# Optimization experiments

Hardware: AMD Instinct MI355X
Metric: run time of the kernel (lower is better)

## Reference

```python
import jax, jax.numpy as jnp
import numpy as np

B, L, D, DIN, A, V, R = 1024, 100, 256, 704, 128, 32000, 129


def setup_inputs() -> dict:
    key = jax.random.key(0)
    ks = jax.random.split(key, 18)
    s = 0.05
    inp = {
        "x": jax.random.normal(ks[0], (B, DIN), jnp.float32),
        "h0": jax.random.normal(ks[1], (B, D), jnp.float32),
        "c0": jax.random.normal(ks[2], (B, D), jnp.float32),
        "src_enc": jax.random.normal(ks[3], (B, L, D), jnp.float32),
        "src_token_ids": jax.random.randint(ks[4], (B, L), 0, V),
        "W_ih": jax.random.normal(ks[5], (4 * D, DIN), jnp.float32) * s,
        "b_ih": jax.random.normal(ks[6], (4 * D,), jnp.float32) * s,
        "W_hh": jax.random.normal(ks[7], (4 * D, D), jnp.float32) * s,
        "b_hh": jax.random.normal(ks[8], (4 * D,), jnp.float32) * s,
        "W_attn": jax.random.normal(ks[9], (D, D), jnp.float32) * s,
        "W_att_vec": jax.random.normal(ks[10], (A * 2, 2 * D), jnp.float32) * s,
        "W_ptr": jax.random.normal(ks[11], (D, D), jnp.float32) * s,
        "rule_emb": jax.random.normal(ks[12], (R, 128), jnp.float32) * s,
        "W_rule_proj": jax.random.normal(ks[13], (D, 128), jnp.float32) * s,
        "prim_emb": jax.random.normal(ks[14], (V, 128), jnp.float32) * s,
        "W_prim_proj": jax.random.normal(ks[15], (D, 128), jnp.float32) * s,
        "w_gen": jax.random.normal(ks[16], (2, D), jnp.float32) * s,
        "b_gen": jax.random.normal(ks[17], (2,), jnp.float32) * s,
    }
    # W_att_vec maps concat(h, ctx) [2D] -> ATT (=256); keep shape (256, 512)
    inp["W_att_vec"] = inp["W_att_vec"][:256]
    return inp


def reference(x, h0, c0, src_enc, src_token_ids, W_ih, b_ih, W_hh, b_hh,
              W_attn, W_att_vec, W_ptr, rule_emb, W_rule_proj,
              prim_emb, W_prim_proj, w_gen, b_gen):
    # --- LSTMCell (torch gate order i, f, g, o) ---
    gates = x @ W_ih.T + b_ih + h0 @ W_hh.T + b_hh          # [B, 4D]
    i, f, g, o = jnp.split(gates, 4, axis=-1)
    i, f, o = jax.nn.sigmoid(i), jax.nn.sigmoid(f), jax.nn.sigmoid(o)
    c = f * c0 + i * jnp.tanh(g)
    h = o * jnp.tanh(c)                                      # [B, D]

    # --- dot-product attention over source encodings ---
    enc_proj = src_enc @ W_attn.T                            # [B, L, D]
    scores = jnp.einsum('bd,bld->bl', h, enc_proj)
    alpha = jax.nn.softmax(scores, axis=-1)
    ctx = jnp.einsum('bl,bld->bd', alpha, src_enc)
    att = jnp.tanh(jnp.concatenate([h, ctx], axis=-1) @ W_att_vec.T)  # [B, 256]

    # --- apply-rule (production) readout ---
    rule_proj = rule_emb @ W_rule_proj.T                     # [R, 256]
    log_p_rule = jax.nn.log_softmax(att @ rule_proj.T, axis=-1)  # [B, R]

    # --- primitive generation readout ---
    prim_proj = prim_emb @ W_prim_proj.T                     # [V, 256]
    p_gen_prim = jax.nn.softmax(att @ prim_proj.T, axis=-1)  # [B, V]

    # --- pointer network copy distribution over source positions ---
    ptr_scores = jnp.einsum('bld,bd->bl', src_enc @ W_ptr.T, att)
    copy_p = jax.nn.softmax(ptr_scores, axis=-1)             # [B, L]

    # --- gen vs copy gate (softmax over 2, per usage in parse()) ---
    gate = jax.nn.softmax(att @ w_gen.T + b_gen, axis=-1)    # [B, 2]

    # --- combined primitive distribution: gen + scattered copy mass ---
    p_prim = gate[:, :1] * p_gen_prim                        # [B, V]
    copy_mass = gate[:, 1:] * copy_p                         # [B, L]
    bidx = jnp.arange(p_prim.shape[0])[:, None]
    p_prim = p_prim.at[bidx, src_token_ids].add(copy_mass)
    return log_p_rule, p_prim, h, c, att
```

## Files before the change

### kernel.cpp

```cpp
#include <hip/hip_runtime.h>
#include <hip/hip_bf16.h>
#include <math.h>

#define NB   1024
#define LL   100
#define DD   256
#define DINN 704
#define VV   32000
#define RR   129
#define KAV  512

typedef float f32x4 __attribute__((ext_vector_type(4)));
typedef short s16x8 __attribute__((ext_vector_type(8)));
typedef unsigned short u16;

__device__ __forceinline__ float sigf(float x) { return 1.0f / (1.0f + __expf(-x)); }

__device__ __forceinline__ u16 f2bf(float f) {
    unsigned int u = __float_as_uint(f);
    u += 0x7fffu + ((u >> 16) & 1u);
    return (u16)(u >> 16);
}
__device__ __forceinline__ float bf2f(u16 s) {
    return __uint_as_float(((unsigned int)s) << 16);
}

__global__ __launch_bounds__(256) void k_lstm(
    const float* __restrict__ x, const float* __restrict__ h0, const float* __restrict__ c0,
    const float* __restrict__ W_ih, const float* __restrict__ b_ih,
    const float* __restrict__ W_hh, const float* __restrict__ b_hh,
    float* __restrict__ out_h, float* __restrict__ out_c)
{
    __shared__ __align__(16) float As[16][36];
    __shared__ __align__(16) float Bs[16][68];
    __shared__ __align__(16) float gsm[32][68];
    const int t = threadIdx.x;
    const int row0 = blockIdx.x * 32;
    const int dg = blockIdx.y;
    const int tr = t >> 4, tc = t & 15;
    float acc[2][4] = {};

    for (int kt = 0; kt < 60; ++kt) {
        const float* __restrict__ Asrc;
        const float* __restrict__ Bsrc;
        int lda, kb;
        if (kt < 44) { Asrc = x;  Bsrc = W_ih; lda = DINN; kb = kt * 16; }
        else         { Asrc = h0; Bsrc = W_hh; lda = DD;   kb = (kt - 44) * 16; }
        __syncthreads();
#pragma unroll
        for (int p = 0; p < 2; ++p) {
            int e = t + p * 256;
            int r = e >> 4, kk = e & 15;
            As[kk][r] = Asrc[(row0 + r) * lda + kb + kk];
        }
#pragma unroll
        for (int p = 0; p < 4; ++p) {
            int e = t + p * 256;
// ... 8 lines not shown
            f32x4 b = *reinterpret_cast<const f32x4*>(&Bs[kk][tc * 4]);
#pragma unroll
            for (int i = 0; i < 4; ++i) {
                acc[0][i] = fmaf(a0, b[i], acc[0][i]);
                acc[1][i] = fmaf(a1, b[i], acc[1][i]);
            }
        }
    }
    __syncthreads();
#pragma unroll
    for (int j = 0; j < 2; ++j)
#pragma unroll
        for (int i = 0; i < 4; ++i)
            gsm[tr * 2 + j][tc * 4 + i] = acc[j][i];
    __syncthreads();

#pragma unroll
    for (int p = 0; p < 2; ++p) {
        int item = t + p * 256;
        int r = item >> 4, di = item & 15;
        int dcol = dg * 16 + di;
        float iv = gsm[r][di]      + b_ih[dcol]          + b_hh[dcol];
        float fv = gsm[r][16 + di] + b_ih[DD + dcol]     + b_hh[DD + dcol];
        float gv = gsm[r][32 + di] + b_ih[2 * DD + dcol] + b_hh[2 * DD + dcol];
        float ov = gsm[r][48 + di] + b_ih[3 * DD + dcol] + b_hh[3 * DD + dcol];
        float cprev = c0[(row0 + r) * DD + dcol];
        float cc = sigf(fv) * cprev + sigf(iv) * tanhf(gv);
        float hh = sigf(ov) * tanhf(cc);
        out_c[(row0 + r) * DD + dcol] = cc;
        out_h[(row0 + r) * DD + dcol] = hh;
    }
}

__global__ __launch_bounds__(256) void k_attn(
    const float* __restrict__ src_enc, const float* __restrict__ h,
    const float* __restrict__ W_attn, float* __restrict__ ctx_out)
{
    __shared__ __align__(16) u16 enc_s[LL * DD];
    __shared__ __align__(16) float h_s[DD];
    __shared__ __align__(16) float hw_s[DD];
    __shared__ float sc_s[LL];
    __shared__ float al_s[LL];
    const int b = blockIdx.x, t = threadIdx.x;
    const int lane = t & 63, w = t >> 6;

    h_s[t] = h[b * DD + t];
    __syncthreads();
    {
        float a0 = 0.f, a1 = 0.f, a2 = 0.f, a3 = 0.f;
        const float* __restrict__ wp = W_attn + t;
#pragma unroll 4
        for (int e = 0; e < DD; e += 4) {
            a0 = fmaf(h_s[e],     wp[(e)     * DD], a0);
            a1 = fmaf(h_s[e + 1], wp[(e + 1) * DD], a1);
            a2 = fmaf(h_s[e + 2], wp[(e + 2) * DD], a2);
            a3 = fmaf(h_s[e + 3], wp[(e + 3) * DD], a3);
        }
        hw_s[t] = (a0 + a1) + (a2 + a3);
    }
    __syncthreads();

    const float* __restrict__ enc = src_enc + (size_t)b * LL * DD;
    f32x4 hw4 = *reinterpret_cast<const f32x4*>(&hw_s[lane * 4]);

    for (int l = w; l < LL; l += 4) {
        f32x4 ev = *reinterpret_cast<const f32x4*>(&enc[l * DD + lane * 4]);
        float pr = hw4[0] * ev[0] + hw4[1] * ev[1] + hw4[2] * ev[2] + hw4[3] * ev[3];
#pragma unroll
        for (int m = 1; m < 64; m <<= 1) pr += __shfl_xor(pr, m);
        if (lane == 0) sc_s[l] = pr;
        u16* es = &enc_s[l * DD + lane * 4];
        es[0] = f2bf(ev[0]); es[1] = f2bf(ev[1]); es[2] = f2bf(ev[2]); es[3] = f2bf(ev[3]);
    }
    __syncthreads();
    if (w == 0) {
        float v0 = sc_s[lane];
        float v1 = (lane + 64 < LL) ? sc_s[lane + 64] : -1e30f;
        float m = fmaxf(v0, v1);
#pragma unroll
        for (int s = 1; s < 64; s <<= 1) m = fmaxf(m, __shfl_xor(m, s));
        float e0 = __expf(v0 - m);
        float e1 = (lane + 64 < LL) ? __expf(v1 - m) : 0.f;
        float ssum = e0 + e1;
#pragma unroll
        for (int s = 1; s < 64; s <<= 1) ssum += __shfl_xor(ssum, s);
        float inv = 1.f / ssum;
        al_s[lane] = e0 * inv;
        if (lane + 64 < LL) al_s[lane + 64] = e1 * inv;
    }
    __syncthreads();
    float accv = 0.f;
    for (int l = 0; l < LL; ++l) accv += al_s[l] * bf2f(enc_s[l * DD + t]);
    ctx_out[b * DD + t] = accv;
}

__global__ __launch_bounds__(256) void k_attvec(
    const float* __restrict__ h, const float* __restrict__ ctx,
    const float* __restrict__ W_att_vec, float* __restrict__ att_out)
{
    __shared__ __align__(16) float As[16][36];
    __shared__ __align__(16) float Bs[16][68];
    const int t = threadIdx.x;
    const int row0 = blockIdx.x * 32;
    const int col0 = blockIdx.y * 64;
    const int tr = t >> 4, tc = t & 15;
    float acc[2][4] = {};
    for (int kt = 0; kt < 32; ++kt) {
        const float* __restrict__ Asrc = (kt < 16) ? h : ctx;
        int kb = (kt < 16) ? kt * 16 : (kt - 16) * 16;
        int kg = kt * 16;
        __syncthreads();
#pragma unroll
        for (int p = 0; p < 2; ++p) {
            int e = t + p * 256;
            int r = e >> 4, kk = e & 15;
            As[kk][r] = Asrc[(row0 + r) * DD + kb + kk];
        }
#pragma unroll
        for (int p = 0; p < 4; ++p) {
            int e = t + p * 256;
            int r = e >> 4, kk = e & 15;
            Bs[kk][r] = W_att_vec[(col0 + r) * KAV + kg + kk];
        }
        __syncthreads();
#pragma unroll
        for (int kk = 0; kk < 16; ++kk) {
            float a0 = As[kk][tr * 2], a1 = As[kk][tr * 2 + 1];
            f32x4 b = *reinterpret_cast<const f32x4*>(&Bs[kk][tc * 4]);
#pragma unroll
            for (int i = 0; i < 4; ++i) {
                acc[0][i] = fmaf(a0, b[i], acc[0][i]);
                acc[1][i] = fmaf(a1, b[i], acc[1][i]);
            }
        }
    }
#pragma unroll
    for (int j = 0; j < 2; ++j)
#pragma unroll
        for (int i = 0; i < 4; ++i)
            att_out[(row0 + tr * 2 + j) * DD + col0 + tc * 4 + i] = tanhf(acc[j][i]);
}

__global__ __launch_bounds__(256) void k_readout(
    const float* __restrict__ att, const float* __restrict__ src_enc,
    const float* __restrict__ rule_proj, const float* __restrict__ W_ptr,
    const float* __restrict__ W_prim_proj, const float* __restrict__ w_gen,
    const float* __restrict__ b_gen,
    float* __restrict__ log_p_rule, u16* __restrict__ att_bf,
    float* __restrict__ gate0_ws, float* __restrict__ copy_mass)
{
    __shared__ __align__(16) float att_s[DD];
    __shared__ __align__(16) float atw_s[DD];
    __shared__ float red_s[RR];
    __shared__ float sc_s[LL];
    __shared__ float gl_s[2];
    __shared__ float mS[2];
    const int b = blockIdx.x, t = threadIdx.x;
    const int lane = t & 63, w = t >> 6;
    att_s[t] = att[b * DD + t];
    __syncthreads();

    if (t < RR) {
        float acc = 0.f;
        const float* __restrict__ rp = &rule_proj[t * DD];
        for (int d = 0; d < DD; d += 4) {
            f32x4 r4 = *reinterpret_cast<const f32x4*>(&rp[d]);
            f32x4 a4 = *reinterpret_cast<const f32x4*>(&att_s[d]);
            acc += r4[0] * a4[0] + r4[1] * a4[1] + r4[2] * a4[2] + r4[3] * a4[3];
        }
        red_s[t] = acc;
    }
    {
        float aw = 0.f;
        for (int d = 0; d < DD; ++d) aw += att_s[d] * W_ptr[d * DD + t];
        atw_s[t] = aw;
    }
    if (t < 128) {
        float ap = 0.f;
        for (int d = 0; d < DD; ++d) ap += att_s[d] * W_prim_proj[d * 128 + t];
        att_bf[b * 128 + t] = f2bf(ap);
    }
    if (w < 2) {
        f32x4 a4 = *reinterpret_cast<const f32x4*>(&att_s[lane * 4]);
        f32x4 g4 = *reinterpret_cast<const f32x4*>(&w_gen[w * DD + lane * 4]);
        float p = a4[0] * g4[0] + a4[1] * g4[1] + a4[2] * g4[2] + a4[3] * g4[3];
#pragma unroll
        for (int s = 1; s < 64; s <<= 1) p += __shfl_xor(p, s);
        if (lane == 0) gl_s[w] = p + b_gen[w];
    }
    __syncthreads();

    if (w == 0) {
        float v0 = red_s[lane];
        float v1 = red_s[lane + 64];
        float v2 = (lane == 0) ? red_s[128] : -1e30f;
        float m = fmaxf(fmaxf(v0, v1), v2);
#pragma unroll
        for (int s = 1; s < 64; s <<= 1) m = fmaxf(m, __shfl_xor(m, s));
        float ssum = __expf(v0 - m) + __expf(v1 - m) + ((lane == 0) ? __expf(v2 - m) : 0.f);
#pragma unroll
        for (int s = 1; s < 64; s <<= 1) ssum += __shfl_xor(ssum, s);
        if (lane == 0) { mS[0] = m; mS[1] = logf(ssum); }
    }
    __syncthreads();
    if (t < RR) log_p_rule[b * RR + t] = red_s[t] - mS[0] - mS[1];

    float g0 = gl_s[0], g1 = gl_s[1];
    float gm = fmaxf(g0, g1);
    float e0 = __expf(g0 - gm), e1 = __expf(g1 - gm);
    float gate1 = e1 / (e0 + e1);
    if (t == 0) gate0_ws[b] = e0 / (e0 + e1);

    const float* __restrict__ enc = src_enc + (size_t)b * LL * DD;
    f32x4 aw4 = *reinterpret_cast<const f32x4*>(&atw_s[lane * 4]);
    for (int l = w; l < LL; l += 4) {
        f32x4 ev = *reinterpret_cast<const f32x4*>(&enc[l * DD + lane * 4]);
        float pr = aw4[0] * ev[0] + aw4[1] * ev[1] + aw4[2] * ev[2] + aw4[3] * ev[3];
#pragma unroll
        for (int m = 1; m < 64; m <<= 1) pr += __shfl_xor(pr, m);
        if (lane == 0) sc_s[l] = pr;
    }
    __syncthreads();
    if (w == 0) {
        float v0 = sc_s[lane];
        float v1 = (lane + 64 < LL) ? sc_s[lane + 64] : -1e30f;
        float m = fmaxf(v0, v1);
#pragma unroll
        for (int s = 1; s < 64; s <<= 1) m = fmaxf(m, __shfl_xor(m, s));
        float ee0 = __expf(v0 - m);
        float ee1 = (lane + 64 < LL) ? __expf(v1 - m) : 0.f;
        float ssum = ee0 + ee1;
#pragma unroll
        for (int s = 1; s < 64; s <<= 1) ssum += __shfl_xor(ssum, s);
        float inv = 1.f / ssum;
        copy_mass[b * LL + lane] = gate1 * ee0 * inv;
        if (lane + 64 < LL) copy_mass[b * LL + lane + 64] = gate1 * ee1 * inv;
    }
}

__global__ __launch_bounds__(256) void k_conv(
    const float* __restrict__ src, u16* __restrict__ dst,
    const float* __restrict__ rule_emb, const float* __restrict__ W_rule_proj,
    float* __restrict__ rule_proj)
{
    __shared__ float re_s[128];
    const int bx = blockIdx.x, t = threadIdx.x;
    if (bx < RR && t < 128) re_s[t] = rule_emb[bx * 128 + t];

    int i = (bx * 256 + t) * 8;
    f32x4 a = *reinterpret_cast<const f32x4*>(&src[i]);
    f32x4 b = *reinterpret_cast<const f32x4*>(&src[i + 4]);
    s16x8 r;
    r[0] = (short)f2bf(a[0]); r[1] = (short)f2bf(a[1]);
    r[2] = (short)f2bf(a[2]); r[3] = (short)f2bf(a[3]);
    r[4] = (short)f2bf(b[0]); r[5] = (short)f2bf(b[1]);
    r[6] = (short)f2bf(b[2]); r[7] = (short)f2bf(b[3]);
    *reinterpret_cast<s16x8*>(&dst[i]) = r;

    if (bx < RR) {
        __syncthreads();
        float acc = 0.f;
        const float* __restrict__ wr = &W_rule_proj[t * 128];
#pragma unroll 8
        for (int k = 0; k < 128; k += 4) {
            f32x4 w4 = *reinterpret_cast<const f32x4*>(&wr[k]);
            acc += w4[0] * re_s[k] + w4[1] * re_s[k + 1]
                 + w4[2] * re_s[k + 2] + w4[3] * re_s[k + 3];
        }
        rule_proj[bx * DD + t] = acc;
    }
}

template <int PASS>
__global__ __launch_bounds__(256) void k_prim(
    const u16* __restrict__ att_bf, const u16* __restrict__ prim_bf,
    const float* __restrict__ coef, float* __restrict__ stats, float* __restrict__ p_prim)
{
    const int t = threadIdx.x;
    const int lane = t & 63, w = t >> 6;
    const int lm = lane & 15, lq = lane >> 4;
    const int colbase = blockIdx.x * 128 + (w & 1) * 64;
    const int chunk = colbase >> 6;
    const int rowblk = blockIdx.y * 256;

    s16x8 pfr[4][4];
#pragma unroll
    for (int kg = 0; kg < 4; ++kg)
#pragma unroll
        for (int mg = 0; mg < 4; ++mg)
            pfr[kg][mg] = *reinterpret_cast<const s16x8*>(
                &prim_bf[(size_t)(colbase + mg * 16 + lm) * 128 + kg * 32 + lq * 8]);

    for (int it = 0; it < 2; ++it) {
        const int rowbase = rowblk + it * 128 + (w >> 1) * 64;
        f32x4 acc[4][4] = {};
#pragma unroll
        for (int kg = 0; kg < 4; ++kg) {
            s16x8 afr[4];
#pragma unroll
            for (int ng = 0; ng < 4; ++ng)
                afr[ng] = *reinterpret_cast<const s16x8*>(
                    &att_bf[(rowbase + ng * 16 + lm) * 128 + kg * 32 + lq * 8]);
// ... 62 lines not shown
}

extern "C" void kernel_launch(void* const* d_in, const int* in_sizes, int n_in,
                              void* d_out, int out_size, void* d_ws, size_t ws_size,
                              hipStream_t stream)
{
    const float* x         = (const float*)d_in[0];
    const float* h0        = (const float*)d_in[1];
    const float* c0        = (const float*)d_in[2];
    const float* src_enc   = (const float*)d_in[3];
    const int*   tok       = (const int*)  d_in[4];
    const float* W_ih      = (const float*)d_in[5];
    const float* b_ih      = (const float*)d_in[6];
    const float* W_hh      = (const float*)d_in[7];
    const float* b_hh      = (const float*)d_in[8];
    const float* W_attn    = (const float*)d_in[9];
    const float* W_att_vec = (const float*)d_in[10];
    const float* W_ptr     = (const float*)d_in[11];
    const float* rule_emb  = (const float*)d_in[12];
    const float* W_rule_pr = (const float*)d_in[13];
    const float* prim_emb  = (const float*)d_in[14];
    const float* W_prim_pr = (const float*)d_in[15];
    const float* w_gen     = (const float*)d_in[16];
    const float* b_gen     = (const float*)d_in[17];

    float* out    = (float*)d_out;
    float* o_logp = out;
    float* o_pp   = out + 1024 * 129;
    float* o_h    = o_pp + (size_t)1024 * 32000;
    float* o_c    = o_h + 1024 * 256;
    float* o_att  = o_c + 1024 * 256;

    float* wsf      = (float*)d_ws;
    float* ws_ctx   = wsf;
    float* ws_rp    = ws_ctx   + 262144;
    float* ws_gate  = ws_rp    + 33280;
    float* ws_cm    = ws_gate  + 1024;
    float* ws_coef  = ws_cm    + 102400;
    float* ws_stats = ws_coef  + 1024;
    u16*   ws_attbf = (u16*)(ws_stats + 512000);
    u16*   ws_primbf= (u16*)(ws_stats + 512000 + 65536);

    k_conv<<<dim3(2000), 256, 0, stream>>>(prim_emb, ws_primbf, rule_emb, W_rule_pr, ws_rp);
    k_lstm<<<dim3(32, 16), 256, 0, stream>>>(x, h0, c0, W_ih, b_ih, W_hh, b_hh, o_h, o_c);
    k_attn<<<dim3(1024), 256, 0, stream>>>(src_enc, o_h, W_attn, ws_ctx);
    k_attvec<<<dim3(32, 4), 256, 0, stream>>>(o_h, ws_ctx, W_att_vec, o_att);
    k_readout<<<dim3(1024), 256, 0, stream>>>(o_att, src_enc, ws_rp, W_ptr, W_prim_pr,
                                              w_gen, b_gen, o_logp, ws_attbf, ws_gate, ws_cm);
    k_prim<0><<<dim3(250, 4), 256, 0, stream>>>(ws_attbf, ws_primbf, nullptr, ws_stats, nullptr);
    k_combine<<<dim3(4), 256, 0, stream>>>(ws_stats, ws_gate, ws_coef);
    k_prim<1><<<dim3(250, 4), 256, 0, stream>>>(ws_attbf, ws_primbf, ws_coef, nullptr, o_pp);
    k_scatter<<<dim3(400), 256, 0, stream>>>(tok, ws_cm, o_pp);
}
```

Baseline: 267.4 us.

## Fuse attention, att-vector projection and readout into one per-batch kernel

Merges k_attn, k_attvec and k_readout into a single per-row kernel. It computes the context vector, the att-vector GEMV, the pointer, prim and rule projections, and the copy softmax while keeping intermediates in shared memory. W_att_vec is pre-transposed by extra blocks appended to k_conv so the per-row GEMV reads are coalesced. The bf16 staging of src_enc in LDS is dropped, and the second and third passes re-read src_enc from global/L2. This saves two launches and the ctx round-trip, but the att-vector projection becomes a per-row GEMV that re-reads the weights for each batch row instead of a tiled GEMM.

```diff
diff --git a/kernel.cpp b/kernel.cpp
--- a/kernel.cpp
+++ b/kernel.cpp
@@ -11,6 +11,7 @@
 #define KAV  512
 
 typedef float f32x4 __attribute__((ext_vector_type(4)));
+typedef float f32x2 __attribute__((ext_vector_type(2)));
 typedef short s16x8 __attribute__((ext_vector_type(8)));
 typedef unsigned short u16;
 
@@ -20,9 +21,6 @@
     unsigned int u = __float_as_uint(f);
     u += 0x7fffu + ((u >> 16) & 1u);
     return (u16)(u >> 16);
-}
-__device__ __forceinline__ float bf2f(u16 s) {
-    return __uint_as_float(((unsigned int)s) << 16);
 }
 
 __global__ __launch_bounds__(256) void k_lstm(
@@ -97,219 +95,31 @@
     }
 }
 
-__global__ __launch_bounds__(256) void k_attn(
-    const float* __restrict__ src_enc, const float* __restrict__ h,
-    const float* __restrict__ W_attn, float* __restrict__ ctx_out)
-{
-    __shared__ __align__(16) u16 enc_s[LL * DD];
-    __shared__ __align__(16) float h_s[DD];
-    __shared__ __align__(16) float hw_s[DD];
-    __shared__ float sc_s[LL];
-    __shared__ float al_s[LL];
-    const int b = blockIdx.x, t = threadIdx.x;
-    const int lane = t & 63, w = t >> 6;
-
-    h_s[t] = h[b * DD + t];
-    __syncthreads();
-    {
-        float a0 = 0.f, a1 = 0.f, a2 = 0.f, a3 = 0.f;
-        const float* __restrict__ wp = W_attn + t;
-#pragma unroll 4
-        for (int e = 0; e < DD; e += 4) {
-            a0 = fmaf(h_s[e],     wp[(e)     * DD], a0);
-            a1 = fmaf(h_s[e + 1], wp[(e + 1) * DD], a1);
-            a2 = fmaf(h_s[e + 2], wp[(e + 2) * DD], a2);
-            a3 = fmaf(h_s[e + 3], wp[(e + 3) * DD], a3);
-        }
-        hw_s[t] = (a0 + a1) + (a2 + a3);
-    }
-    __syncthreads();
-
-    const float* __restrict__ enc = src_enc + (size_t)b * LL * DD;
-    f32x4 hw4 = *reinterpret_cast<const f32x4*>(&hw_s[lane * 4]);
-
-    for (int l = w; l < LL; l += 4) {
-        f32x4 ev = *reinterpret_cast<const f32x4*>(&enc[l * DD + lane * 4]);
-        float pr = hw4[0] * ev[0] + hw4[1] * ev[1] + hw4[2] * ev[2] + hw4[3] * ev[3];
-#pragma unroll
-        for (int m = 1; m < 64; m <<= 1) pr += __shfl_xor(pr, m);
-        if (lane == 0) sc_s[l] = pr;
-        u16* es = &enc_s[l * DD + lane * 4];
-        es[0] = f2bf(ev[0]); es[1] = f2bf(ev[1]); es[2] = f2bf(ev[2]); es[3] = f2bf(ev[3]);
-    }
-    __syncthreads();
-    if (w == 0) {
-        float v0 = sc_s[lane];
-        float v1 = (lane + 64 < LL) ? sc_s[lane + 64] : -1e30f;
-        float m = fmaxf(v0, v1);
-#pragma unroll
-        for (int s = 1; s < 64; s <<= 1) m = fmaxf(m, __shfl_xor(m, s));
-        float e0 = __expf(v0 - m);
-        float e1 = (lane + 64 < LL) ? __expf(v1 - m) : 0.f;
-        float ssum = e0 + e1;
-#pragma unroll
-        for (int s = 1; s < 64; s <<= 1) ssum += __shfl_xor(ssum, s);
-        float inv = 1.f / ssum;
-        al_s[lane] = e0 * inv;
-        if (lane + 64 < LL) al_s[lane + 64] = e1 * inv;
-    }
-    __syncthreads();
-    float accv = 0.f;
-    for (int l = 0; l < LL; ++l) accv += al_s[l] * bf2f(enc_s[l * DD + t]);
-    ctx_out[b * DD + t] = accv;
-}
-
-__global__ __launch_bounds__(256) void k_attvec(
-    const float* __restrict__ h, const float* __restrict__ ctx,
-    const float* __restrict__ W_att_vec, float* __restrict__ att_out)
-{
-    __shared__ __align__(16) float As[16][36];
-    __shared__ __align__(16) float Bs[16][68];
-    const int t = threadIdx.x;
-    const int row0 = blockIdx.x * 32;
-    const int col0 = blockIdx.y * 64;
-    const int tr = t >> 4, tc = t & 15;
-    float acc[2][4] = {};
-    for (int kt = 0; kt < 32; ++kt) {
-        const float* __restrict__ Asrc = (kt < 16) ? h : ctx;
-        int kb = (kt < 16) ? kt * 16 : (kt - 16) * 16;
-        int kg = kt * 16;
-        __syncthreads();
-#pragma unroll
-        for (int p = 0; p < 2; ++p) {
-            int e = t + p * 256;
-            int r = e >> 4, kk = e & 15;
-            As[kk][r] = Asrc[(row0 + r) * DD + kb + kk];
-        }
-#pragma unroll
-        for (int p = 0; p < 4; ++p) {
-            int e = t + p * 256;
-            int r = e >> 4, kk = e & 15;
-            Bs[kk][r] = W_att_vec[(col0 + r) * KAV + kg + kk];
-        }
-        __syncthreads();
-#pragma unroll
-        for (int kk = 0; kk < 16; ++kk) {
-            float a0 = As[kk][tr * 2], a1 = As[kk][tr * 2 + 1];
-            f32x4 b = *reinterpret_cast<const f32x4*>(&Bs[kk][tc * 4]);
-#pragma unroll
-            for (int i = 0; i < 4; ++i) {
-                acc[0][i] = fmaf(a0, b[i], acc[0][i]);
-                acc[1][i] = fmaf(a1, b[i], acc[1][i]);
-            }
-        }
-    }
-#pragma unroll
-    for (int j = 0; j < 2; ++j)
-#pragma unroll
-        for (int i = 0; i < 4; ++i)
-            att_out[(row0 + tr * 2 + j) * DD + col0 + tc * 4 + i] = tanhf(acc[j][i]);
-}
-
-__global__ __launch_bounds__(256) void k_readout(
-    const float* __restrict__ att, const float* __restrict__ src_enc,
-    const float* __restrict__ rule_proj, const float* __restrict__ W_ptr,
-    const float* __restrict__ W_prim_proj, const float* __restrict__ w_gen,
-    const float* __restrict__ b_gen,
-    float* __restrict__ log_p_rule, u16* __restrict__ att_bf,
-    float* __restrict__ gate0_ws, float* __restrict__ copy_mass)
-{
-    __shared__ __align__(16) float att_s[DD];
-    __shared__ __align__(16) float atw_s[DD];
-    __shared__ float red_s[RR];
-    __shared__ float sc_s[LL];
-    __shared__ float gl_s[2];
-    __shared__ float mS[2];
-    const int b = blockIdx.x, t = threadIdx.x;
-    const int lane = t & 63, w = t >> 6;
-    att_s[t] = att[b * DD + t];
-    __syncthreads();
-
-    if (t < RR) {
-        float acc = 0.f;
-        const float* __restrict__ rp = &rule_proj[t * DD];
-        for (int d = 0; d < DD; d += 4) {
-            f32x4 r4 = *reinterpret_cast<const f32x4*>(&rp[d]);
-            f32x4 a4 = *reinterpret_cast<const f32x4*>(&att_s[d]);
-            acc += r4[0] * a4[0] + r4[1] * a4[1] + r4[2] * a4[2] + r4[3] * a4[3];
-        }
-        red_s[t] = acc;
-    }
-    {
-        float aw = 0.f;
-        for (int d = 0; d < DD; ++d) aw += att_s[d] * W_ptr[d * DD + t];
-        atw_s[t] = aw;
-    }
-    if (t < 128) {
-        float ap = 0.f;
-        for (int d = 0; d < DD; ++d) ap += att_s[d] * W_prim_proj[d * 128 + t];
-        att_bf[b * 128 + t] = f2bf(ap);
-    }
-    if (w < 2) {
-        f32x4 a4 = *reinterpret_cast<const f32x4*>(&att_s[lane * 4]);
-        f32x4 g4 = *reinterpret_cast<const f32x4*>(&w_gen[w * DD + lane * 4]);
-        float p = a4[0] * g4[0] + a4[1] * g4[1] + a4[2] * g4[2] + a4[3] * g4[3];
-#pragma unroll
-        for (int s = 1; s < 64; s <<= 1) p += __shfl_xor(p, s);
-        if (lane == 0) gl_s[w] = p + b_gen[w];
-    }
-    __syncthreads();
-
-    if (w == 0) {
-        float v0 = red_s[lane];
-        float v1 = red_s[lane + 64];
-        float v2 = (lane == 0) ? red_s[128] : -1e30f;
-        float m = fmaxf(fmaxf(v0, v1), v2);
-#pragma unroll
-        for (int s = 1; s < 64; s <<= 1) m = fmaxf(m, __shfl_xor(m, s));
-        float ssum = __expf(v0 - m) + __expf(v1 - m) + ((lane == 0) ? __expf(v2 - m) : 0.f);
-#pragma unroll
-        for (int s = 1; s < 64; s <<= 1) ssum += __shfl_xor(ssum, s);
-        if (lane == 0) { mS[0] = m; mS[1] = logf(ssum); }
-    }
-    __syncthreads();
-    if (t < RR) log_p_rule[b * RR + t] = red_s[t] - mS[0] - mS[1];
-
-    float g0 = gl_s[0], g1 = gl_s[1];
-    float gm = fmaxf(g0, g1);
-    float e0 = __expf(g0 - gm), e1 = __expf(g1 - gm);
-    float gate1 = e1 / (e0 + e1);
-    if (t == 0) gate0_ws[b] = e0 / (e0 + e1);
-
-    const float* __restrict__ enc = src_enc + (size_t)b * LL * DD;
-    f32x4 aw4 = *reinterpret_cast<const f32x4*>(&atw_s[lane * 4]);
-    for (int l = w; l < LL; l += 4) {
-        f32x4 ev = *reinterpret_cast<const f32x4*>(&enc[l * DD + lane * 4]);
-        float pr = aw4[0] * ev[0] + aw4[1] * ev[1] + aw4[2] * ev[2] + aw4[3] * ev[3];
-#pragma unroll
-        for (int m = 1; m < 64; m <<= 1) pr += __shfl_xor(pr, m);
-        if (lane == 0) sc_s[l] = pr;
-    }
-    __syncthreads();
-    if (w == 0) {
-        float v0 = sc_s[lane];
-        float v1 = (lane + 64 < LL) ? sc_s[lane + 64] : -1e30f;
-        float m = fmaxf(v0, v1);
-#pragma unroll
-        for (int s = 1; s < 64; s <<= 1) m = fmaxf(m, __shfl_xor(m, s));
-        float ee0 = __expf(v0 - m);
-        float ee1 = (lane + 64 < LL) ? __expf(v1 - m) : 0.f;
-        float ssum = ee0 + ee1;
-#pragma unroll
-        for (int s = 1; s < 64; s <<= 1) ssum += __shfl_xor(ssum, s);
-        float inv = 1.f / ssum;
-        copy_mass[b * LL + lane] = gate1 * ee0 * inv;
-        if (lane + 64 < LL) copy_mass[b * LL + lane + 64] = gate1 * ee1 * inv;
-    }
-}
-
 __global__ __launch_bounds__(256) void k_conv(
     const float* __restrict__ src, u16* __restrict__ dst,
     const float* __restrict__ rule_emb, const float* __restrict__ W_rule_proj,
-    float* __restrict__ rule_proj)
+    float* __restrict__ rule_proj,
+    const float* __restrict__ W_att_vec, float* __restrict__ wt)
 {
     __shared__ float re_s[128];
+    __shared__ __align__(16) float tile[64][65];
     const int bx = blockIdx.x, t = threadIdx.x;
+
+    if (bx >= 2000) {
+        const int id = bx - 2000;
+        const int c0 = (id >> 3) * 64;
+        const int k0 = (id & 7) * 64;
+        const int r = t >> 6, cc = t & 63;
+#pragma unroll
+        for (int p = 0; p < 16; ++p)
+            tile[r + p * 4][cc] = W_att_vec[(c0 + r + p * 4) * KAV + k0 + cc];
+        __syncthreads();
+#pragma unroll
+        for (int p = 0; p < 16; ++p)
+            wt[(k0 + r + p * 4) * DD + c0 + cc] = tile[cc][r + p * 4];
+        return;
+    }
+
     if (bx < RR && t < 128) re_s[t] = rule_emb[bx * 128 + t];
 
     int i = (bx * 256 + t) * 8;
@@ -333,6 +143,223 @@
                  + w4[2] * re_s[k + 2] + w4[3] * re_s[k + 3];
         }
         rule_proj[bx * DD + t] = acc;
+    }
+}
+
+__global__ __launch_bounds__(256) void k_fused(
+    const float* __restrict__ src_enc, const float* __restrict__ h,
+    const float* __restrict__ W_attn, const float* __restrict__ Wt,
+    const float* __restrict__ rule_proj, const float* __restrict__ W_ptr,
+    const float* __restrict__ W_prim_proj, const float* __restrict__ w_gen,
+    const float* __restrict__ b_gen,
+    float* __restrict__ att_out, float* __restrict__ log_p_rule,
+    u16* __restrict__ att_bf, float* __restrict__ gate0_ws,
+    float* __restrict__ copy_mass)
+{
+    __shared__ __align__(16) float hc_s[2 * DD];
+    __shared__ __align__(16) float att_s[DD];
+    __shared__ __align__(16) float part[4][DD];
+    __shared__ __align__(16) float partp[4][128];
+    __shared__ float sc_s[LL];
+    __shared__ float al_s[LL];
+    __shared__ float red_s[RR];
+    __shared__ float gl_s[2];
+    __shared__ float mS[2];
+
+    const int b = blockIdx.x, t = threadIdx.x;
+    const int lane = t & 63, w = t >> 6;
+    const float* __restrict__ enc = src_enc + (size_t)b * LL * DD;
+
+    hc_s[t] = h[b * DD + t];
+    __syncthreads();
+
+    {
+        f32x4 p = {0.f, 0.f, 0.f, 0.f};
+        const int e0 = w * 64;
+#pragma unroll 4
+        for (int e = e0; e < e0 + 64; ++e) {
+            float hv = hc_s[e];
+            f32x4 wv = *reinterpret_cast<const f32x4*>(&W_attn[e * DD + lane * 4]);
+            p[0] = fmaf(hv, wv[0], p[0]); p[1] = fmaf(hv, wv[1], p[1]);
+            p[2] = fmaf(hv, wv[2], p[2]); p[3] = fmaf(hv, wv[3], p[3]);
+        }
+        *reinterpret_cast<f32x4*>(&part[w][lane * 4]) = p;
+    }
+    __syncthreads();
+    f32x4 hw4;
+    {
+        f32x4 p0 = *reinterpret_cast<const f32x4*>(&part[0][lane * 4]);
+        f32x4 p1 = *reinterpret_cast<const f32x4*>(&part[1][lane * 4]);
+        f32x4 p2 = *reinterpret_cast<const f32x4*>(&part[2][lane * 4]);
+        f32x4 p3 = *reinterpret_cast<const f32x4*>(&part[3][lane * 4]);
+        hw4[0] = (p0[0] + p1[0]) + (p2[0] + p3[0]);
+        hw4[1] = (p0[1] + p1[1]) + (p2[1] + p3[1]);
+        hw4[2] = (p0[2] + p1[2]) + (p2[2] + p3[2]);
+        hw4[3] = (p0[3] + p1[3]) + (p2[3] + p3[3]);
+    }
+
+    for (int l = w; l < LL; l += 4) {
+        f32x4 ev = *reinterpret_cast<const f32x4*>(&enc[l * DD + lane * 4]);
+        float pr = hw4[0] * ev[0] + hw4[1] * ev[1] + hw4[2] * ev[2] + hw4[3] * ev[3];
+#pragma unroll
+        for (int m = 1; m < 64; m <<= 1) pr += __shfl_xor(pr, m);
+        if (lane == 0) sc_s[l] = pr;
+    }
+    __syncthreads();
+    if (w == 0) {
+        float v0 = sc_s[lane];
+        float v1 = (lane + 64 < LL) ? sc_s[lane + 64] : -1e30f;
+        float m = fmaxf(v0, v1);
+#pragma unroll
+        for (int s = 1; s < 64; s <<= 1) m = fmaxf(m, __shfl_xor(m, s));
+        float e0 = __expf(v0 - m);
+        float e1 = (lane + 64 < LL) ? __expf(v1 - m) : 0.f;
+        float ssum = e0 + e1;
+#pragma unroll
+        for (int s = 1; s < 64; s <<= 1) ssum += __shfl_xor(ssum, s);
+        float inv = 1.f / ssum;
+        al_s[lane] = e0 * inv;
+        if (lane + 64 < LL) al_s[lane + 64] = e1 * inv;
+    }
+    __syncthreads();
+
+    {
+        float a0 = 0.f, a1 = 0.f, a2 = 0.f, a3 = 0.f;
+        for (int l = 0; l < LL; l += 4) {
+            a0 = fmaf(al_s[l],     enc[(l)     * DD + t], a0);
+            a1 = fmaf(al_s[l + 1], enc[(l + 1) * DD + t], a1);
+            a2 = fmaf(al_s[l + 2], enc[(l + 2) * DD + t], a2);
+            a3 = fmaf(al_s[l + 3], enc[(l + 3) * DD + t], a3);
+        }
+        hc_s[DD + t] = (a0 + a1) + (a2 + a3);
+    }
+    __syncthreads();
+
+    {
+        f32x4 p = {0.f, 0.f, 0.f, 0.f};
+        const int gk0 = w * 128;
+#pragma unroll 4
+        for (int kk = 0; kk < 128; ++kk) {
+            float cv = hc_s[gk0 + kk];
+            f32x4 wv = *reinterpret_cast<const f32x4*>(&Wt[(gk0 + kk) * DD + lane * 4]);
+            p[0] = fmaf(cv, wv[0], p[0]); p[1] = fmaf(cv, wv[1], p[1]);
+            p[2] = fmaf(cv, wv[2], p[2]); p[3] = fmaf(cv, wv[3], p[3]);
+        }
+        *reinterpret_cast<f32x4*>(&part[w][lane * 4]) = p;
+    }
+    __syncthreads();
+    {
+        float av = (part[0][t] + part[1][t]) + (part[2][t] + part[3][t]);
+        av = tanhf(av);
+        att_s[t] = av;
+        att_out[b * DD + t] = av;
+    }
+    __syncthreads();
+
+    {
+        f32x4 p = {0.f, 0.f, 0.f, 0.f};
+        const int e0 = w * 64;
+#pragma unroll 4
+        for (int e = e0; e < e0 + 64; ++e) {
+            float av = att_s[e];
+            f32x4 wv = *reinterpret_cast<const f32x4*>(&W_ptr[e * DD + lane * 4]);
+            p[0] = fmaf(av, wv[0], p[0]); p[1] = fmaf(av, wv[1], p[1]);
+            p[2] = fmaf(av, wv[2], p[2]); p[3] = fmaf(av, wv[3], p[3]);
+        }
+        *reinterpret_cast<f32x4*>(&part[w][lane * 4]) = p;
+    }
+    {
+        float p0 = 0.f, p1 = 0.f;
+        const int e0 = w * 64;
+#pragma unroll 4
+        for (int e = e0; e < e0 + 64; ++e) {
+            float av = att_s[e];
+            f32x2 wv = *reinterpret_cast<const f32x2*>(&W_prim_proj[e * 128 + lane * 2]);
+            p0 = fmaf(av, wv[0], p0);
+            p1 = fmaf(av, wv[1], p1);
+        }
+        partp[w][lane * 2]     = p0;
+        partp[w][lane * 2 + 1] = p1;
+    }
+    if (t < RR) {
+        float acc = 0.f;
+        const float* __restrict__ rp = &rule_proj[t * DD];
+#pragma unroll 4
+        for (int d = 0; d < DD; d += 4) {
+            f32x4 r4 = *reinterpret_cast<const f32x4*>(&rp[d]);
+            f32x4 a4 = *reinterpret_cast<const f32x4*>(&att_s[d]);
+            acc += r4[0] * a4[0] + r4[1] * a4[1] + r4[2] * a4[2] + r4[3] * a4[3];
+        }
+        red_s[t] = acc;
+    }
+    if (w < 2) {
+        f32x4 a4 = *reinterpret_cast<const f32x4*>(&att_s[lane * 4]);
+        f32x4 g4 = *reinterpret_cast<const f32x4*>(&w_gen[w * DD + lane * 4]);
+        float p = a4[0] * g4[0] + a4[1] * g4[1] + a4[2] * g4[2] + a4[3] * g4[3];
+#pragma unroll
+        for (int s = 1; s < 64; s <<= 1) p += __shfl_xor(p, s);
+        if (lane == 0) gl_s[w] = p + b_gen[w];
+    }
+    __syncthreads();
+
+    f32x4 aw4;
+    {
+        f32x4 p0 = *reinterpret_cast<const f32x4*>(&part[0][lane * 4]);
+        f32x4 p1 = *reinterpret_cast<const f32x4*>(&part[1][lane * 4]);
+        f32x4 p2 = *reinterpret_cast<const f32x4*>(&part[2][lane * 4]);
+        f32x4 p3 = *reinterpret_cast<const f32x4*>(&part[3][lane * 4]);
+        aw4[0] = (p0[0] + p1[0]) + (p2[0] + p3[0]);
+        aw4[1] = (p0[1] + p1[1]) + (p2[1] + p3[1]);
+        aw4[2] = (p0[2] + p1[2]) + (p2[2] + p3[2]);
+        aw4[3] = (p0[3] + p1[3]) + (p2[3] + p3[3]);
+    }
+    if (t < 128) {
+        float ap = (partp[0][t] + partp[1][t]) + (partp[2][t] + partp[3][t]);
+        att_bf[b * 128 + t] = f2bf(ap);
+    }
+    if (w == 0) {
+        float v0 = red_s[lane];
+        float v1 = red_s[lane + 64];
+        float v2 = (lane == 0) ? red_s[128] : -1e30f;
+        float m = fmaxf(fmaxf(v0, v1), v2);
+#pragma unroll
+        for (int s = 1; s < 64; s <<= 1) m = fmaxf(m, __shfl_xor(m, s));
+        float ssum = __expf(v0 - m) + __expf(v1 - m) + ((lane == 0) ? __expf(v2 - m) : 0.f);
+#pragma unroll
+        for (int s = 1; s < 64; s <<= 1) ssum += __shfl_xor(ssum, s);
+        if (lane == 0) { mS[0] = m; mS[1] = logf(ssum); }
+    }
+    __syncthreads();
+    if (t < RR) log_p_rule[b * RR + t] = red_s[t] - mS[0] - mS[1];
+
+    float g0 = gl_s[0], g1 = gl_s[1];
+    float gm = fmaxf(g0, g1);
+    float e0g = __expf(g0 - gm), e1g = __expf(g1 - gm);
+    float gate1 = e1g / (e0g + e1g);
+    if (t == 0) gate0_ws[b] = e0g / (e0g + e1g);
+
+    for (int l = w; l < LL; l += 4) {
+        f32x4 ev = *reinterpret_cast<const f32x4*>(&enc[l * DD + lane * 4]);
+        float pr = aw4[0] * ev[0] + aw4[1] * ev[1] + aw4[2] * ev[2] + aw4[3] * ev[3];
+#pragma unroll
+        for (int m = 1; m < 64; m <<= 1) pr += __shfl_xor(pr, m);
+        if (lane == 0) sc_s[l] = pr;
+    }
+    __syncthreads();
+    if (w == 0) {
+        float v0 = sc_s[lane];
+        float v1 = (lane + 64 < LL) ? sc_s[lane + 64] : -1e30f;
+        float m = fmaxf(v0, v1);
+#pragma unroll
+        for (int s = 1; s < 64; s <<= 1) m = fmaxf(m, __shfl_xor(m, s));
+        float ee0 = __expf(v0 - m);
+        float ee1 = (lane + 64 < LL) ? __expf(v1 - m) : 0.f;
+        float ssum = ee0 + ee1;
+#pragma unroll
+        for (int s = 1; s < 64; s <<= 1) ssum += __shfl_xor(ssum, s);
+        float inv = 1.f / ssum;
+        copy_mass[b * LL + lane] = gate1 * ee0 * inv;
+        if (lane + 64 < LL) copy_mass[b * LL + lane + 64] = gate1 * ee1 * inv;
     }
 }
 
@@ -461,21 +488,21 @@
     float* o_att  = o_c + 1024 * 256;
 
     float* wsf      = (float*)d_ws;
-    float* ws_ctx   = wsf;
-    float* ws_rp    = ws_ctx   + 262144;
+    float* ws_rp    = wsf;
     float* ws_gate  = ws_rp    + 33280;
     float* ws_cm    = ws_gate  + 1024;
     float* ws_coef  = ws_cm    + 102400;
     float* ws_stats = ws_coef  + 1024;
-    u16*   ws_attbf = (u16*)(ws_stats + 512000);
-    u16*   ws_primbf= (u16*)(ws_stats + 512000 + 65536);
-
-    k_conv<<<dim3(2000), 256, 0, stream>>>(prim_emb, ws_primbf, rule_emb, W_rule_pr, ws_rp);
+    float* ws_wt    = ws_stats + 512000;
+    u16*   ws_attbf = (u16*)(ws_wt + 131072);
+    u16*   ws_primbf= (u16*)(ws_wt + 131072 + 65536);
+
+    k_conv<<<dim3(2032), 256, 0, stream>>>(prim_emb, ws_primbf, rule_emb, W_rule_pr,
+                                           ws_rp, W_att_vec, ws_wt);
     k_lstm<<<dim3(32, 16), 256, 0, stream>>>(x, h0, c0, W_ih, b_ih, W_hh, b_hh, o_h, o_c);
-    k_attn<<<dim3(1024), 256, 0, stream>>>(src_enc, o_h, W_attn, ws_ctx);
-    k_attvec<<<dim3(32, 4), 256, 0, stream>>>(o_h, ws_ctx, W_att_vec, o_att);
-    k_readout<<<dim3(1024), 256, 0, stream>>>(o_att, src_enc, ws_rp, W_ptr, W_prim_pr,
-                                              w_gen, b_gen, o_logp, ws_attbf, ws_gate, ws_cm);
+    k_fused<<<dim3(1024), 256, 0, stream>>>(src_enc, o_h, W_attn, ws_wt, ws_rp, W_ptr,
+                                            W_prim_pr, w_gen, b_gen,
+                                            o_att, o_logp, ws_attbf, ws_gate, ws_cm);
     k_prim<0><<<dim3(250, 4), 256, 0, stream>>>(ws_attbf, ws_primbf, nullptr, ws_stats, nullptr);
     k_combine<<<dim3(4), 256, 0, stream>>>(ws_stats, ws_gate, ws_coef);
     k_prim<1><<<dim3(250, 4), 256, 0, stream>>>(ws_attbf, ws_primbf, ws_coef, nullptr, o_pp);
```

New measurement: 249.8 us. -6.6%, faster.

## Batch per-row matvecs into tiled GEMMs and restructure attention kernel

Applied to the files above, without the earlier changes.

The per-batch-row matrix-vector products (h·W_attn, att·W_ptr, att·W_prim_proj) move out of the per-row kernels into tiled GEMM kernels, so each weight tile is reused across 32 rows instead of being reread by every block. The attention kernel now stages the bf16 encodings in padded shared memory first, then computes scores and the context with a split-over-L reduction. The readout splits into a rule/gate kernel and a pointer kernel. This adds extra launches and workspace round trips in exchange for removing redundant weight traffic.

```diff
diff --git a/kernel.cpp b/kernel.cpp
--- a/kernel.cpp
+++ b/kernel.cpp
@@ -9,20 +9,23 @@
 #define VV   32000
 #define RR   129
 #define KAV  512
+#define ROWU 129
 
 typedef float f32x4 __attribute__((ext_vector_type(4)));
+typedef float f32x2 __attribute__((ext_vector_type(2)));
 typedef short s16x8 __attribute__((ext_vector_type(8)));
 typedef unsigned short u16;
+typedef unsigned int u32;
 
 __device__ __forceinline__ float sigf(float x) { return 1.0f / (1.0f + __expf(-x)); }
 
 __device__ __forceinline__ u16 f2bf(float f) {
-    unsigned int u = __float_as_uint(f);
+    u32 u = __float_as_uint(f);
     u += 0x7fffu + ((u >> 16) & 1u);
     return (u16)(u >> 16);
 }
 __device__ __forceinline__ float bf2f(u16 s) {
-    return __uint_as_float(((unsigned int)s) << 16);
+    return __uint_as_float(((u32)s) << 16);
 }
 
 __global__ __launch_bounds__(256) void k_lstm(
@@ -97,47 +100,132 @@
     }
 }
 
-__global__ __launch_bounds__(256) void k_attn(
-    const float* __restrict__ src_enc, const float* __restrict__ h,
-    const float* __restrict__ W_attn, float* __restrict__ ctx_out)
-{
-    __shared__ __align__(16) u16 enc_s[LL * DD];
-    __shared__ __align__(16) float h_s[DD];
+__global__ __launch_bounds__(256) void k_conv(
+    const float* __restrict__ src, u16* __restrict__ dst,
+    const float* __restrict__ rule_emb, const float* __restrict__ W_rule_proj,
+    float* __restrict__ rule_proj)
+{
+    __shared__ float re_s[128];
+    const int bx = blockIdx.x, t = threadIdx.x;
+
+    if (bx < RR && t < 128) re_s[t] = rule_emb[bx * 128 + t];
+
+    int i = (bx * 256 + t) * 8;
+    f32x4 a = *reinterpret_cast<const f32x4*>(&src[i]);
+    f32x4 b = *reinterpret_cast<const f32x4*>(&src[i + 4]);
+    s16x8 r;
+    r[0] = (short)f2bf(a[0]); r[1] = (short)f2bf(a[1]);
+    r[2] = (short)f2bf(a[2]); r[3] = (short)f2bf(a[3]);
+    r[4] = (short)f2bf(b[0]); r[5] = (short)f2bf(b[1]);
+    r[6] = (short)f2bf(b[2]); r[7] = (short)f2bf(b[3]);
+    *reinterpret_cast<s16x8*>(&dst[i]) = r;
+
+    if (bx < RR) {
+        __syncthreads();
+        float acc = 0.f;
+        const float* __restrict__ wr = &W_rule_proj[t * 128];
+#pragma unroll 8
+        for (int k = 0; k < 128; k += 4) {
+            f32x4 w4 = *reinterpret_cast<const f32x4*>(&wr[k]);
+            acc += w4[0] * re_s[k] + w4[1] * re_s[k + 1]
+                 + w4[2] * re_s[k + 2] + w4[3] * re_s[k + 3];
+        }
+        rule_proj[bx * DD + t] = acc;
+    }
+}
+
+__global__ __launch_bounds__(256) void k_hw(
+    const float* __restrict__ h, const float* __restrict__ W_attn, float* __restrict__ hW)
+{
+    __shared__ __align__(16) float As[16][36];
+    __shared__ __align__(16) float Bs[16][68];
+    const int t = threadIdx.x;
+    const int row0 = blockIdx.x * 32;
+    const int col0 = blockIdx.y * 64;
+    const int tr = t >> 4, tc = t & 15;
+    float acc[2][4] = {};
+    for (int kt = 0; kt < 16; ++kt) {
+        __syncthreads();
+#pragma unroll
+        for (int p = 0; p < 2; ++p) {
+            int e = t + p * 256;
+            int r = e >> 4, kk = e & 15;
+            As[kk][r] = h[(row0 + r) * DD + kt * 16 + kk];
+        }
+#pragma unroll
+        for (int p = 0; p < 4; ++p) {
+            int e = t + p * 256;
+            int kk = e >> 6, c = e & 63;
+            Bs[kk][c] = W_attn[(kt * 16 + kk) * DD + col0 + c];
+        }
+        __syncthreads();
+#pragma unroll
+        for (int kk = 0; kk < 16; ++kk) {
+            float a0 = As[kk][tr * 2], a1 = As[kk][tr * 2 + 1];
+            f32x4 b = *reinterpret_cast<const f32x4*>(&Bs[kk][tc * 4]);
+#pragma unroll
+            for (int i = 0; i < 4; ++i) {
+                acc[0][i] = fmaf(a0, b[i], acc[0][i]);
+                acc[1][i] = fmaf(a1, b[i], acc[1][i]);
+            }
+        }
+    }
+#pragma unroll
+    for (int j = 0; j < 2; ++j) {
+        f32x4 v;
+#pragma unroll
+        for (int i = 0; i < 4; ++i) v[i] = acc[j][i];
+        *reinterpret_cast<f32x4*>(&hW[(row0 + tr * 2 + j) * DD + col0 + tc * 4]) = v;
+    }
+}
+
+__global__ __launch_bounds__(256) void k_attn2(
+    const float* __restrict__ src_enc, const float* __restrict__ hW,
+    float* __restrict__ ctx_out)
+{
+    __shared__ u32 enc_u[LL * ROWU];
+    __shared__ __align__(16) float part[4][DD];
     __shared__ __align__(16) float hw_s[DD];
     __shared__ float sc_s[LL];
     __shared__ float al_s[LL];
+
     const int b = blockIdx.x, t = threadIdx.x;
     const int lane = t & 63, w = t >> 6;
-
-    h_s[t] = h[b * DD + t];
-    __syncthreads();
+    const float* __restrict__ enc = src_enc + (size_t)b * LL * DD;
+
+    hw_s[t] = hW[b * DD + t];
+
+#pragma unroll 5
+    for (int p = 0; p < 25; ++p) {
+        int q = p * 256 + t;
+        int l = q >> 6, dq = q & 63;
+        f32x4 ev = *reinterpret_cast<const f32x4*>(&enc[l * DD + dq * 4]);
+        u32 w0 = (u32)f2bf(ev[0]) | ((u32)f2bf(ev[1]) << 16);
+        u32 w1 = (u32)f2bf(ev[2]) | ((u32)f2bf(ev[3]) << 16);
+        enc_u[l * ROWU + dq * 2]     = w0;
+        enc_u[l * ROWU + dq * 2 + 1] = w1;
+    }
+    __syncthreads();
+
     {
-        float a0 = 0.f, a1 = 0.f, a2 = 0.f, a3 = 0.f;
-        const float* __restrict__ wp = W_attn + t;
-#pragma unroll 4
-        for (int e = 0; e < DD; e += 4) {
-            a0 = fmaf(h_s[e],     wp[(e)     * DD], a0);
-            a1 = fmaf(h_s[e + 1], wp[(e + 1) * DD], a1);
-            a2 = fmaf(h_s[e + 2], wp[(e + 2) * DD], a2);
-            a3 = fmaf(h_s[e + 3], wp[(e + 3) * DD], a3);
-        }
-        hw_s[t] = (a0 + a1) + (a2 + a3);
-    }
-    __syncthreads();
-
-    const float* __restrict__ enc = src_enc + (size_t)b * LL * DD;
-    f32x4 hw4 = *reinterpret_cast<const f32x4*>(&hw_s[lane * 4]);
-
-    for (int l = w; l < LL; l += 4) {
-        f32x4 ev = *reinterpret_cast<const f32x4*>(&enc[l * DD + lane * 4]);
-        float pr = hw4[0] * ev[0] + hw4[1] * ev[1] + hw4[2] * ev[2] + hw4[3] * ev[3];
-#pragma unroll
-        for (int m = 1; m < 64; m <<= 1) pr += __shfl_xor(pr, m);
-        if (lane == 0) sc_s[l] = pr;
-        u16* es = &enc_s[l * DD + lane * 4];
-        es[0] = f2bf(ev[0]); es[1] = f2bf(ev[1]); es[2] = f2bf(ev[2]); es[3] = f2bf(ev[3]);
-    }
-    __syncthreads();
+        const int sl = ((w >> 1) << 6) + lane;
+        float sp = 0.f;
+        if (sl < LL) {
+            const u32* __restrict__ rp = enc_u + sl * ROWU + ((w & 1) << 6);
+            const float* __restrict__ hp = hw_s + ((w & 1) << 7);
+#pragma unroll 16
+            for (int k = 0; k < 64; ++k) {
+                u32 v = rp[k];
+                sp = fmaf(bf2f((u16)v),         hp[2 * k],     sp);
+                sp = fmaf(bf2f((u16)(v >> 16)), hp[2 * k + 1], sp);
+            }
+        }
+        part[w][lane] = sp;
+    }
+    __syncthreads();
+    if (t < LL) sc_s[t] = part[(t >> 6) << 1][t & 63] + part[((t >> 6) << 1) + 1][t & 63];
+    __syncthreads();
+
     if (w == 0) {
         float v0 = sc_s[lane];
         float v1 = (lane + 64 < LL) ? sc_s[lane + 64] : -1e30f;
@@ -154,12 +242,29 @@
         if (lane + 64 < LL) al_s[lane + 64] = e1 * inv;
     }
     __syncthreads();
-    float accv = 0.f;
-    for (int l = 0; l < LL; ++l) accv += al_s[l] * bf2f(enc_s[l * DD + t]);
-    ctx_out[b * DD + t] = accv;
-}
-
-__global__ __launch_bounds__(256) void k_attvec(
+
+    {
+        const int l0 = w * 25;
+        float c0 = 0.f, c1 = 0.f, c2 = 0.f, c3 = 0.f;
+#pragma unroll 5
+        for (int li = 0; li < 25; ++li) {
+            int l = l0 + li;
+            float a = al_s[l];
+            u32 v0 = enc_u[l * ROWU + lane * 2];
+            u32 v1 = enc_u[l * ROWU + lane * 2 + 1];
+            c0 = fmaf(a, bf2f((u16)v0), c0);
+            c1 = fmaf(a, bf2f((u16)(v0 >> 16)), c1);
+            c2 = fmaf(a, bf2f((u16)v1), c2);
+            c3 = fmaf(a, bf2f((u16)(v1 >> 16)), c3);
+        }
+        f32x4 p; p[0] = c0; p[1] = c1; p[2] = c2; p[3] = c3;
+        *reinterpret_cast<f32x4*>(&part[w][lane * 4]) = p;
+    }
+    __syncthreads();
+    ctx_out[b * DD + t] = (part[0][t] + part[1][t]) + (part[2][t] + part[3][t]);
+}
+
+__global__ __launch_bounds__(256) void k_att(
     const float* __restrict__ h, const float* __restrict__ ctx,
     const float* __restrict__ W_att_vec, float* __restrict__ att_out)
 {
@@ -206,18 +311,71 @@
             att_out[(row0 + tr * 2 + j) * DD + col0 + tc * 4 + i] = tanhf(acc[j][i]);
 }
 
-__global__ __launch_bounds__(256) void k_readout(
-    const float* __restrict__ att, const float* __restrict__ src_enc,
-    const float* __restrict__ rule_proj, const float* __restrict__ W_ptr,
-    const float* __restrict__ W_prim_proj, const float* __restrict__ w_gen,
-    const float* __restrict__ b_gen,
-    float* __restrict__ log_p_rule, u16* __restrict__ att_bf,
-    float* __restrict__ gate0_ws, float* __restrict__ copy_mass)
+__global__ __launch_bounds__(256) void k_ptrproj(
+    const float* __restrict__ att, const float* __restrict__ W_ptr,
+    const float* __restrict__ W_prim_proj,
+    float* __restrict__ atw, u16* __restrict__ att_bf)
+{
+    __shared__ __align__(16) float As[16][36];
+    __shared__ __align__(16) float Bs[16][68];
+    const int t = threadIdx.x;
+    const int row0 = blockIdx.x * 32;
+    const int col0 = blockIdx.y * 64;
+    const int tr = t >> 4, tc = t & 15;
+    float acc[2][4] = {};
+    for (int kt = 0; kt < 16; ++kt) {
+        __syncthreads();
+#pragma unroll
+        for (int p = 0; p < 2; ++p) {
+            int e = t + p * 256;
+            int r = e >> 4, kk = e & 15;
+            As[kk][r] = att[(row0 + r) * DD + kt * 16 + kk];
+        }
+#pragma unroll
+        for (int p = 0; p < 4; ++p) {
+            int e = t + p * 256;
+            int kk = e >> 6, c = e & 63;
+            Bs[kk][c] = (col0 < 256)
+                ? W_ptr[(kt * 16 + kk) * DD + col0 + c]
+                : W_prim_proj[(kt * 16 + kk) * 128 + (col0 - 256) + c];
+        }
+        __syncthreads();
+#pragma unroll
+        for (int kk = 0; kk < 16; ++kk) {
+            float a0 = As[kk][tr * 2], a1 = As[kk][tr * 2 + 1];
+            f32x4 b = *reinterpret_cast<const f32x4*>(&Bs[kk][tc * 4]);
+#pragma unroll
+            for (int i = 0; i < 4; ++i) {
+                acc[0][i] = fmaf(a0, b[i], acc[0][i]);
+                acc[1][i] = fmaf(a1, b[i], acc[1][i]);
+            }
+        }
+    }
+    if (col0 < 256) {
+#pragma unroll
+        for (int j = 0; j < 2; ++j) {
+            f32x4 v;
+#pragma unroll
+            for (int i = 0; i < 4; ++i) v[i] = acc[j][i];
+            *reinterpret_cast<f32x4*>(&atw[(row0 + tr * 2 + j) * DD + col0 + tc * 4]) = v;
+        }
+    } else {
+#pragma unroll
+        for (int j = 0; j < 2; ++j)
+#pragma unroll
+            for (int i = 0; i < 4; ++i)
+                att_bf[(row0 + tr * 2 + j) * 128 + (col0 - 256) + tc * 4 + i] = f2bf(acc[j][i]);
+    }
+}
+
+__global__ __launch_bounds__(256) void k_rulegate(
+    const float* __restrict__ att, const float* __restrict__ rule_proj,
+    const float* __restrict__ w_gen, const float* __restrict__ b_gen,
+    float* __restrict__ log_p_rule, float* __restrict__ gate0_ws,
+    float* __restrict__ gate1_ws)
 {
     __shared__ __align__(16) float att_s[DD];
-    __shared__ __align__(16) float atw_s[DD];
     __shared__ float red_s[RR];
-    __shared__ float sc_s[LL];
     __shared__ float gl_s[2];
     __shared__ float mS[2];
     const int b = blockIdx.x, t = threadIdx.x;
@@ -228,22 +386,13 @@
     if (t < RR) {
         float acc = 0.f;
         const float* __restrict__ rp = &rule_proj[t * DD];
+#pragma unroll 4
         for (int d = 0; d < DD; d += 4) {
             f32x4 r4 = *reinterpret_cast<const f32x4*>(&rp[d]);
             f32x4 a4 = *reinterpret_cast<const f32x4*>(&att_s[d]);
             acc += r4[0] * a4[0] + r4[1] * a4[1] + r4[2] * a4[2] + r4[3] * a4[3];
         }
         red_s[t] = acc;
-    }
-    {
-        float aw = 0.f;
-        for (int d = 0; d < DD; ++d) aw += att_s[d] * W_ptr[d * DD + t];
-        atw_s[t] = aw;
-    }
-    if (t < 128) {
-        float ap = 0.f;
-        for (int d = 0; d < DD; ++d) ap += att_s[d] * W_prim_proj[d * 128 + t];
-        att_bf[b * 128 + t] = f2bf(ap);
     }
     if (w < 2) {
         f32x4 a4 = *reinterpret_cast<const f32x4*>(&att_s[lane * 4]);
@@ -270,14 +419,25 @@
     __syncthreads();
     if (t < RR) log_p_rule[b * RR + t] = red_s[t] - mS[0] - mS[1];
 
-    float g0 = gl_s[0], g1 = gl_s[1];
-    float gm = fmaxf(g0, g1);
-    float e0 = __expf(g0 - gm), e1 = __expf(g1 - gm);
-    float gate1 = e1 / (e0 + e1);
-    if (t == 0) gate0_ws[b] = e0 / (e0 + e1);
-
+    if (t == 0) {
+        float g0 = gl_s[0], g1 = gl_s[1];
+        float gm = fmaxf(g0, g1);
+        float e0g = __expf(g0 - gm), e1g = __expf(g1 - gm);
+        gate0_ws[b] = e0g / (e0g + e1g);
+        gate1_ws[b] = e1g / (e0g + e1g);
+    }
+}
+
+__global__ __launch_bounds__(256) void k_ptr2(
+    const float* __restrict__ src_enc, const float* __restrict__ atw,
+    const float* __restrict__ gate1_ws, float* __restrict__ copy_mass)
+{
+    __shared__ float sc_s[LL];
+    const int b = blockIdx.x, t = threadIdx.x;
+    const int lane = t & 63, w = t >> 6;
     const float* __restrict__ enc = src_enc + (size_t)b * LL * DD;
-    f32x4 aw4 = *reinterpret_cast<const f32x4*>(&atw_s[lane * 4]);
+    f32x4 aw4 = *reinterpret_cast<const f32x4*>(&atw[b * DD + lane * 4]);
+
     for (int l = w; l < LL; l += 4) {
         f32x4 ev = *reinterpret_cast<const f32x4*>(&enc[l * DD + lane * 4]);
         float pr = aw4[0] * ev[0] + aw4[1] * ev[1] + aw4[2] * ev[2] + aw4[3] * ev[3];
@@ -287,6 +447,7 @@
     }
     __syncthreads();
     if (w == 0) {
+        float gate1 = gate1_ws[b];
         float v0 = sc_s[lane];
         float v1 = (lane + 64 < LL) ? sc_s[lane + 64] : -1e30f;
         float m = fmaxf(v0, v1);
@@ -300,39 +461,6 @@
         float inv = 1.f / ssum;
         copy_mass[b * LL + lane] = gate1 * ee0 * inv;
         if (lane + 64 < LL) copy_mass[b * LL + lane + 64] = gate1 * ee1 * inv;
-    }
-}
-
-__global__ __launch_bounds__(256) void k_conv(
-    const float* __restrict__ src, u16* __restrict__ dst,
-    const float* __restrict__ rule_emb, const float* __restrict__ W_rule_proj,
-    float* __restrict__ rule_proj)
-{
-    __shared__ float re_s[128];
-    const int bx = blockIdx.x, t = threadIdx.x;
-    if (bx < RR && t < 128) re_s[t] = rule_emb[bx * 128 + t];
-
-    int i = (bx * 256 + t) * 8;
-    f32x4 a = *reinterpret_cast<const f32x4*>(&src[i]);
-    f32x4 b = *reinterpret_cast<const f32x4*>(&src[i + 4]);
-    s16x8 r;
-    r[0] = (short)f2bf(a[0]); r[1] = (short)f2bf(a[1]);
-    r[2] = (short)f2bf(a[2]); r[3] = (short)f2bf(a[3]);
-    r[4] = (short)f2bf(b[0]); r[5] = (short)f2bf(b[1]);
-    r[6] = (short)f2bf(b[2]); r[7] = (short)f2bf(b[3]);
-    *reinterpret_cast<s16x8*>(&dst[i]) = r;
-
-    if (bx < RR) {
-        __syncthreads();
-        float acc = 0.f;
-        const float* __restrict__ wr = &W_rule_proj[t * 128];
-#pragma unroll 8
-        for (int k = 0; k < 128; k += 4) {
-            f32x4 w4 = *reinterpret_cast<const f32x4*>(&wr[k]);
-            acc += w4[0] * re_s[k] + w4[1] * re_s[k + 1]
-                 + w4[2] * re_s[k + 2] + w4[3] * re_s[k + 3];
-        }
-        rule_proj[bx * DD + t] = acc;
     }
 }
 
@@ -461,23 +589,29 @@
     float* o_att  = o_c + 1024 * 256;
 
     float* wsf      = (float*)d_ws;
-    float* ws_ctx   = wsf;
-    float* ws_rp    = ws_ctx   + 262144;
-    float* ws_gate  = ws_rp    + 33280;
-    float* ws_cm    = ws_gate  + 1024;
+    float* ws_rp    = wsf;
+    float* ws_gate0 = ws_rp    + 33280;
+    float* ws_gate1 = ws_gate0 + 1024;
+    float* ws_cm    = ws_gate1 + 1024;
     float* ws_coef  = ws_cm    + 102400;
-    float* ws_stats = ws_coef  + 1024;
+    float* ws_hw    = ws_coef  + 1024;
+    float* ws_ctx   = ws_hw    + 262144;
+    float* ws_atw   = ws_ctx   + 262144;
+    float* ws_stats = ws_atw   + 262144;
     u16*   ws_attbf = (u16*)(ws_stats + 512000);
     u16*   ws_primbf= (u16*)(ws_stats + 512000 + 65536);
 
     k_conv<<<dim3(2000), 256, 0, stream>>>(prim_emb, ws_primbf, rule_emb, W_rule_pr, ws_rp);
     k_lstm<<<dim3(32, 16), 256, 0, stream>>>(x, h0, c0, W_ih, b_ih, W_hh, b_hh, o_h, o_c);
-    k_attn<<<dim3(1024), 256, 0, stream>>>(src_enc, o_h, W_attn, ws_ctx);
-    k_attvec<<<dim3(32, 4), 256, 0, stream>>>(o_h, ws_ctx, W_att_vec, o_att);
-    k_readout<<<dim3(1024), 256, 0, stream>>>(o_att, src_enc, ws_rp, W_ptr, W_prim_pr,
-                                              w_gen, b_gen, o_logp, ws_attbf, ws_gate, ws_cm);
+    k_hw<<<dim3(32, 4), 256, 0, stream>>>(o_h, W_attn, ws_hw);
+    k_attn2<<<dim3(1024), 256, 0, stream>>>(src_enc, ws_hw, ws_ctx);
+    k_att<<<dim3(32, 4), 256, 0, stream>>>(o_h, ws_ctx, W_att_vec, o_att);
+    k_ptrproj<<<dim3(32, 6), 256, 0, stream>>>(o_att, W_ptr, W_prim_pr, ws_atw, ws_attbf);
+    k_rulegate<<<dim3(1024), 256, 0, stream>>>(o_att, ws_rp, w_gen, b_gen,
+                                               o_logp, ws_gate0, ws_gate1);
+    k_ptr2<<<dim3(1024), 256, 0, stream>>>(src_enc, ws_atw, ws_gate1, ws_cm);
     k_prim<0><<<dim3(250, 4), 256, 0, stream>>>(ws_attbf, ws_primbf, nullptr, ws_stats, nullptr);
-    k_combine<<<dim3(4), 256, 0, stream>>>(ws_stats, ws_gate, ws_coef);
+    k_combine<<<dim3(4), 256, 0, stream>>>(ws_stats, ws_gate0, ws_coef);
     k_prim<1><<<dim3(250, 4), 256, 0, stream>>>(ws_attbf, ws_primbf, ws_coef, nullptr, o_pp);
     k_scatter<<<dim3(400), 256, 0, stream>>>(tok, ws_cm, o_pp);
 }
```

After: 259.4 us. 1.03x faster.
